# Kernel tuning notes

Hardware: AMD Instinct MI355X
Metric: run time of the kernel (lower is better)

Reference implementation:

```python
import jax, jax.numpy as jnp
import numpy as np

N, A, OBS, H, E, ITERS = 2000, 16, 64, 128, 16000, 8


def _init_linear(key, din, dout):
    kw, kb = jax.random.split(key)
    s = 1.0 / np.sqrt(din)
    W = jax.random.uniform(kw, (dout, din), minval=-s, maxval=s, dtype=jnp.float32)
    b = jax.random.uniform(kb, (dout,), minval=-s, maxval=s, dtype=jnp.float32)
    return W, b


def setup_inputs() -> dict:
    key = jax.random.key(0)
    ks = jax.random.split(key, 20)
    x = jax.random.normal(ks[0], (N, OBS), dtype=jnp.float32)
    prev_action = jax.random.normal(ks[1], (N, A), dtype=jnp.float32)
    state = jax.random.normal(ks[2], (1, N, H), dtype=jnp.float32)
    # edges: unique-ish random pairs with i < j (no self loops)
    rng = np.random.default_rng(0)
    ei = rng.integers(0, N - 1, size=E)
    ej = rng.integers(ei + 1, N)
    edges = jnp.asarray(np.stack([ei, ej], axis=1), dtype=jnp.int32)
    # GRU params (torch layout: rows = [r; z; n])
    s = 1.0 / np.sqrt(H)
    gru_wih = jax.random.uniform(ks[3], (3 * H, OBS + A), minval=-s, maxval=s, dtype=jnp.float32)
    gru_whh = jax.random.uniform(ks[4], (3 * H, H), minval=-s, maxval=s, dtype=jnp.float32)
    gru_bih = jax.random.uniform(ks[5], (3 * H,), minval=-s, maxval=s, dtype=jnp.float32)
    gru_bhh = jax.random.uniform(ks[6], (3 * H,), minval=-s, maxval=s, dtype=jnp.float32)
    # utility MLP: [H, 256, 256, A]
    uW0, ub0 = _init_linear(ks[7], H, 256)
    uW1, ub1 = _init_linear(ks[8], 256, 256)
    uW2, ub2 = _init_linear(ks[9], 256, A)
    # payoff MLP: [2H, H, 256, 256, A, A*A]  (faithful to source's dim-list reuse)
    pW0, pb0 = _init_linear(ks[10], 2 * H, H)
    pW1, pb1 = _init_linear(ks[11], H, 256)
    pW2, pb2 = _init_linear(ks[12], 256, 256)
    pW3, pb3 = _init_linear(ks[13], 256, A)
    pW4, pb4 = _init_linear(ks[14], A, A * A)
    return dict(x=x, prev_action=prev_action, state=state, edges=edges,
                gru_wih=gru_wih, gru_whh=gru_whh, gru_bih=gru_bih, gru_bhh=gru_bhh,
                uW0=uW0, ub0=ub0, uW1=uW1, ub1=ub1, uW2=uW2, ub2=ub2,
                pW0=pW0, pb0=pb0, pW1=pW1, pb1=pb1, pW2=pW2, pb2=pb2,
                pW3=pW3, pb3=pb3, pW4=pW4, pb4=pb4)


def _mlp(x, params):
    n = len(params)
    for i, (W, b) in enumerate(params):
        x = x @ W.T + b
        if i < n - 1:
            x = jax.nn.relu(x)
    return x


def _gru_step(inp, h, wih, whh, bih, bhh):
    gi = inp @ wih.T + bih          # [N, 3H]
    gh = h @ whh.T + bhh            # [N, 3H]
    gir, giz, gin = jnp.split(gi, 3, axis=-1)
    ghr, ghz, ghn = jnp.split(gh, 3, axis=-1)
    r = jax.nn.sigmoid(gir + ghr)
    z = jax.nn.sigmoid(giz + ghz)
    n = jnp.tanh(gin + r * ghn)
    return (1.0 - z) * n + z * h


def _message_passing(u, p, ei, ej):
    """u: [N,A] differentiable, p: [E,A,A] differentiable.
    Messages are computed under stop_gradient (torch.no_grad in source);
    Q of the per-iteration greedy action is differentiable in u, p."""
    u_sg = jax.lax.stop_gradient(u)
    p_sg = jax.lax.stop_gradient(p)
    node_idx = jnp.arange(N)
    edge_idx = jnp.arange(E)

    def step(carry, _):
        M, q_max, opt_a = carry            # M[recv, send, A]
        S = M.sum(axis=1)                  # [N, A] total incoming per node
        base_i = u_sg[ei] + S[ei] - M[ei, ej]   # [E, A] indexed by a_i
        base_j = u_sg[ej] + S[ej] - M[ej, ei]   # [E, A] indexed by a_j
        # message i -> j: max over a_i of (p[e,ai,aj] + base_i[ai])
        msg_to_j = (p_sg + base_i[:, :, None]).max(axis=1)   # [E, A]
        msg_to_j = msg_to_j - msg_to_j.mean(axis=-1, keepdims=True)
        # message j -> i (source reduces over dim 0 = a_i; replicated faithfully)
        msg_to_i = (p_sg + base_j[:, None, :]).max(axis=1)   # [E, A]
        msg_to_i = msg_to_i - msg_to_i.mean(axis=-1, keepdims=True)
        M = M.at[ej, ei].set(msg_to_j).at[ei, ej].set(msg_to_i)
        # greedy action per node
        a_idx = jnp.argmax(u_sg + M.sum(axis=1), axis=-1)    # [N]
        q_real = u[node_idx, a_idx].sum() + p[edge_idx, a_idx[ei], a_idx[ej]].sum()
        better = q_real > q_max
        q_max = jnp.where(better, q_real, q_max)
        a_onehot = jax.nn.one_hot(a_idx, A, dtype=u.dtype)
        opt_a = jnp.where(better, a_onehot, opt_a)
        return (M, q_max, opt_a), None

    M0 = jnp.zeros((N, N, A), dtype=u.dtype)
    q0 = jnp.zeros((), dtype=u.dtype)
    a0 = jnp.zeros((N, A), dtype=u.dtype)
    (M, q_max, opt_a), _ = jax.lax.scan(step, (M0, q0, a0), None, length=ITERS)
    return opt_a, q_max


def reference(x, prev_action, state, edges,
              gru_wih, gru_whh, gru_bih, gru_bhh,
              uW0, ub0, uW1, ub1, uW2, ub2,
              pW0, pb0, pW1, pb1, pW2, pb2, pW3, pb3, pW4, pb4):
    ei, ej = edges[:, 0], edges[:, 1]
    enc_in = jnp.concatenate([x, prev_action], axis=-1)        # [N, OBS+A]
    h = _gru_step(enc_in, state[0], gru_wih, gru_whh, gru_bih, gru_bhh)  # [N, H]
    state_out = h.reshape(1, 1, N, H)
    u_params = [(uW0, ub0), (uW1, ub1), (uW2, ub2)]
    p_params = [(pW0, pb0), (pW1, pb1), (pW2, pb2), (pW3, pb3), (pW4, pb4)]
    u = _mlp(h, u_params) / N                                  # [N, A]
    s_ij = jnp.concatenate([h[ei], h[ej]], axis=-1)            # [E, 2H]
    s_ji = jnp.concatenate([h[ej], h[ei]], axis=-1)
    p_ij = _mlp(s_ij, p_params).reshape(E, A, A) / E
    p_ji = _mlp(s_ji, p_params).reshape(E, A, A) / E
    p = 0.5 * (p_ij + p_ji)                                    # [E, A, A]
    a, q_max = _message_passing(u, p, ei, ej)
    return (a, q_max, u[None], p, state_out)
```

## Files before the change

### kernel.cpp

```cpp
#include <hip/hip_runtime.h>
#include <math.h>

#define N_NODES 2000
#define NA 16
#define NOBS 64
#define NH 128
#define NE 16000
#define NITERS 8

#define WS_MSG       0
#define WS_FLAGS     300000
#define WS_Q         512000
#define WS_SBUF      512016
#define WS_AIDX      800016
#define WS_W         816016
#define WS_PT        832016
#define WS_GIT       (WS_PT + 4000000)
#define WS_GHT       (WS_GIT + 30720)
#define WS_WB        4928016
#define WS_UW0T      (WS_WB + 0)
#define WS_UWCAT     (WS_WB + 32768)
#define WS_UW1T      (WS_WB + 65536)
#define WS_UW2T      (WS_WB + 131072)
#define WS_CAB       (WS_WB + 241664)

#define F16_W1H 0
#define F16_W1L 32768
#define F16_W2H 65536
#define F16_W2L 131072
#define F16_W3H 196608
#define F16_W3L 200704
#define F16_W4H 204800
#define F16_W4L 212992

#define NBLK 500

typedef _Float16 half8 __attribute__((ext_vector_type(8)));
typedef float f32x4 __attribute__((ext_vector_type(4)));

__global__ __launch_bounds__(256) void setup_kernel(
    float* __restrict__ ws, const int* __restrict__ edges,
    const float* __restrict__ uW0, const float* __restrict__ uW1,
    const float* __restrict__ uW2, const float* __restrict__ pW0,
    const float* __restrict__ pW1, const float* __restrict__ pW2,
    const float* __restrict__ pW3, const float* __restrict__ pW4,
    const float* __restrict__ gwih, const float* __restrict__ gwhh)
{
    if (blockIdx.x >= 1024) {
        int e = (blockIdx.x - 1024) * 256 + threadIdx.x;
        if (e < NE) {
            int i = edges[2 * e], j = edges[2 * e + 1];
            ((int*)(ws + WS_PT))[i * N_NODES + j] = -1;
        }
        return;
    }
    const int total = 341904;
    for (int idx = blockIdx.x * 256 + threadIdx.x; idx < total;
         idx += 1024 * 256) {
        if (idx < 16) {
            ws[WS_Q + idx] = 0.f;
        } else {
            int t = idx - 16;
            if (t < 135168) {
                float v;
                if (t < 32768) {
                    int k = t / 256, o = t % 256;
                    v = uW0[o * 128 + k];
                } else if (t < 65536) {
                    int q = t - 32768, k = q / 256, o = q % 256;
                    v = (o < 128) ? pW0[o * 256 + k]
                                  : pW0[(o - 128) * 256 + 128 + k];
                } else if (t < 131072) {
                    int q = t - 65536, k = q / 256, o = q % 256;
                    v = uW1[o * 256 + k];
                } else {
                    int q = t - 131072, k = q / 16, o = q % 16;
                    v = uW2[o * 256 + k];
                }
                ws[WS_WB + t] = v;
            } else if (t < 215056) {
                int q = t - 135168;
                if (q < 30720) {
                    int k4 = q / 1536, r = q % 1536, g = r >> 2, c = r & 3;
                    ws[WS_GIT + q] = gwih[g * 80 + 4 * k4 + c];
                } else if (q < 79872) {
                    int q2 = q - 30720;
                    int k4 = q2 / 1536, r = q2 % 1536, g = r >> 2, c = r & 3;
                    ws[WS_GHT + q2] = gwhh[g * 128 + 4 * k4 + c];
                }
            } else if (t < 325648) {
                int q = t - 215056;
                if (q >= 110592) continue;
                _Float16* fw = (_Float16*)ws;
                float v; int hoff, loff;
                if (q < 32768) {
                    v = pW1[q]; hoff = F16_W1H + q; loff = F16_W1L + q;
                } else if (q < 98304) {
                    int z = q - 32768; v = pW2[z];
                    hoff = F16_W2H + z; loff = F16_W2L + z;
                } else if (q < 102400) {
                    int z = q - 98304; v = pW3[z];
                    hoff = F16_W3H + z; loff = F16_W3L + z;
                } else {
                    int z = q - 102400; int n = z >> 5, kk = z & 31;
                    v = (kk < 16) ? pW4[n * 16 + kk] : 0.f;
                    hoff = F16_W4H + z; loff = F16_W4L + z;
                }
                _Float16 hv = (_Float16)v;
                fw[hoff] = hv;
                fw[loff] = (_Float16)(v - (float)hv);
            } else {
                int qf = t - 325648;
                ((int*)(ws + WS_FLAGS))[qf] = 0;
            }
        }
    }
}

__global__ __launch_bounds__(256) void gru_kernel(
    const float* __restrict__ x, const float* __restrict__ pa,
    const float* __restrict__ st, const float* __restrict__ wihT,
    const float* __restrict__ whhT, const float* __restrict__ bih,
    const float* __restrict__ bhh, float* __restrict__ h_out,
    const int* __restrict__ edges, int* __restrict__ owner)
{
    if (blockIdx.x >= 250) {
        int e = (blockIdx.x - 250) * 256 + threadIdx.x;
        if (e < NE) {
            int i = edges[2 * e], j = edges[2 * e + 1];
            atomicMax(&owner[i * N_NODES + j], e);
        }
        return;
    }
    __shared__ float enc[8][80];
    __shared__ float hp[8][128];
    __shared__ float gi[8][384];
    __shared__ float gh[8][384];
    const int tid = threadIdx.x;
    const int n0 = blockIdx.x * 8;

    for (int idx = tid; idx < 8 * 80; idx += 256) {
        int r = idx / 80, c = idx % 80;
        enc[r][c] = (c < 64) ? x[(n0 + r) * 64 + c] : pa[(n0 + r) * 16 + (c - 64)];
    }
    for (int idx = tid; idx < 8 * 128; idx += 256) {
        int r = idx >> 7, c = idx & 127;
        hp[r][c] = st[(n0 + r) * 128 + c];
    }
    __syncthreads();

    for (int idx = tid; idx < 8 * 384; idx += 256) {
        int g = idx % 384, r = idx / 384;
        float s1 = bih[g];
        #pragma unroll 5
        for (int k4 = 0; k4 < 20; ++k4) {
            const float4 ev = *(const float4*)&enc[r][4 * k4];
            const float4 wv = *(const float4*)&wihT[k4 * 1536 + g * 4];
            s1 = fmaf(ev.x, wv.x, fmaf(ev.y, wv.y, fmaf(ev.z, wv.z, fmaf(ev.w, wv.w, s1))));
        }
        gi[r][g] = s1;
        float s2 = bhh[g];
        #pragma unroll 8
        for (int k4 = 0; k4 < 32; ++k4) {
            const float4 hv = *(const float4*)&hp[r][4 * k4];
            const float4 wv = *(const float4*)&whhT[k4 * 1536 + g * 4];
            s2 = fmaf(hv.x, wv.x, fmaf(hv.y, wv.y, fmaf(hv.z, wv.z, fmaf(hv.w, wv.w, s2))));
        }
        gh[r][g] = s2;
    }
    __syncthreads();

    for (int idx = tid; idx < 8 * 128; idx += 256) {
        int r = idx >> 7, c = idx & 127;
        float rr = 1.f / (1.f + expf(-(gi[r][c] + gh[r][c])));
        float zz = 1.f / (1.f + expf(-(gi[r][128 + c] + gh[r][128 + c])));
        float nn = tanhf(gi[r][256 + c] + rr * gh[r][256 + c]);
        h_out[(n0 + r) * 128 + c] = (1.f - zz) * nn + zz * hp[r][c];
    }
}

__global__ __launch_bounds__(256) void umlp_kernel(
    const float* __restrict__ h, const float* __restrict__ w0t,
    const float* __restrict__ b0, const float* __restrict__ w1t,
    const float* __restrict__ b1, const float* __restrict__ w2t,
    const float* __restrict__ b2, const float* __restrict__ wcat,
    float* __restrict__ u_out, float* __restrict__ Sbuf,
    float* __restrict__ cab, const int* __restrict__ edges,
    const int* __restrict__ owner, int* __restrict__ wflag)
{
    if (blockIdx.x >= 500) {
        int e = (blockIdx.x - 500) * 256 + threadIdx.x;
        if (e < NE) {
            int i = edges[2 * e], j = edges[2 * e + 1];
            wflag[e] = (owner[i * N_NODES + j] == e) ? 1 : 0;
        }
        return;
    }
    __shared__ float A[8][128];
    __shared__ float B[8][256];
    const int tid = threadIdx.x;
    const bool is_cab = blockIdx.x >= 250;
    const int n0 = (is_cab ? blockIdx.x - 250 : blockIdx.x) * 8;

    for (int idx = tid; idx < 8 * 128; idx += 256) {
        int r = idx >> 7, c = idx & 127;
        A[r][c] = h[(n0 + r) * 128 + c];
    }
    __syncthreads();

    if (is_cab) {
        const int o = tid;
        const float* wp = wcat + o;
        float wA[4], wB[4];
        #pragma unroll
        for (int c = 0; c < 4; ++c) wA[c] = wp[c * 256];
        float acc[8];
        #pragma unroll
        for (int r = 0; r < 8; ++r) acc[r] = 0.f;
        for (int k4 = 0; k4 < 32; k4 += 2) {
            #pragma unroll
            for (int c = 0; c < 4; ++c) wB[c] = wp[(4 * (k4 + 1) + c) * 256];
            #pragma unroll
            for (int r = 0; r < 8; ++r) {
                const float4 av = *(const float4*)&A[r][4 * k4];
                acc[r] = fmaf(av.x, wA[0], fmaf(av.y, wA[1], fmaf(av.z, wA[2], fmaf(av.w, wA[3], acc[r]))));
            }
            #pragma unroll
            for (int c = 0; c < 4; ++c) wA[c] = wp[(4 * (k4 + 2) + c) * 256];
            #pragma unroll
            for (int r = 0; r < 8; ++r) {
                const float4 av = *(const float4*)&A[r][4 * k4 + 4];
                acc[r] = fmaf(av.x, wB[0], fmaf(av.y, wB[1], fmaf(av.z, wB[2], fmaf(av.w, wB[3], acc[r]))));
            }
        }
        #pragma unroll
        for (int r = 0; r < 8; ++r) cab[(n0 + r) * 256 + o] = acc[r];
        return;
    }

    {
        const int o = tid;
        const float* wp = w0t + o;
        float wA[4], wB[4];
        #pragma unroll
        for (int c = 0; c < 4; ++c) wA[c] = wp[c * 256];
        float acc[8];
        #pragma unroll
        for (int r = 0; r < 8; ++r) acc[r] = b0[o];
        for (int k4 = 0; k4 < 32; k4 += 2) {
            #pragma unroll
            for (int c = 0; c < 4; ++c) wB[c] = wp[(4 * (k4 + 1) + c) * 256];
            #pragma unroll
            for (int r = 0; r < 8; ++r) {
                const float4 av = *(const float4*)&A[r][4 * k4];
                acc[r] = fmaf(av.x, wA[0], fmaf(av.y, wA[1], fmaf(av.z, wA[2], fmaf(av.w, wA[3], acc[r]))));
            }
            #pragma unroll
            for (int c = 0; c < 4; ++c) wA[c] = wp[(4 * (k4 + 2) + c) * 256];
            #pragma unroll
            for (int r = 0; r < 8; ++r) {
                const float4 av = *(const float4*)&A[r][4 * k4 + 4];
                acc[r] = fmaf(av.x, wB[0], fmaf(av.y, wB[1], fmaf(av.z, wB[2], fmaf(av.w, wB[3], acc[r]))));
            }
        }
        #pragma unroll
        for (int r = 0; r < 8; ++r) B[r][o] = fmaxf(acc[r], 0.f);
    }
    __syncthreads();
    {
        const int o = tid;
        const float* wp = w1t + o;
        float wA[4], wB[4];
        #pragma unroll
        for (int c = 0; c < 4; ++c) wA[c] = wp[c * 256];
        float acc[8];
        #pragma unroll
        for (int r = 0; r < 8; ++r) acc[r] = b1[o];
        for (int k4 = 0; k4 < 64; k4 += 2) {
            #pragma unroll
            for (int c = 0; c < 4; ++c) wB[c] = wp[(4 * (k4 + 1) + c) * 256];
            #pragma unroll
            for (int r = 0; r < 8; ++r) {
                const float4 av = *(const float4*)&B[r][4 * k4];
                acc[r] = fmaf(av.x, wA[0], fmaf(av.y, wA[1], fmaf(av.z, wA[2], fmaf(av.w, wA[3], acc[r]))));
            }
            #pragma unroll
            for (int c = 0; c < 4; ++c) wA[c] = wp[(4 * (k4 + 2) + c) * 256];
            #pragma unroll
            for (int r = 0; r < 8; ++r) {
                const float4 av = *(const float4*)&B[r][4 * k4 + 4];
                acc[r] = fmaf(av.x, wB[0], fmaf(av.y, wB[1], fmaf(av.z, wB[2], fmaf(av.w, wB[3], acc[r]))));
            }
        }
        __syncthreads();
        #pragma unroll
        for (int r = 0; r < 8; ++r) B[r][o] = fmaxf(acc[r], 0.f);
    }
    __syncthreads();
    if (tid < 128) {
        int r = tid >> 4, o = tid & 15;
        float acc = b2[o];
        for (int k4 = 0; k4 < 64; ++k4) {
            const float4 av = *(const float4*)&B[r][4 * k4];
            acc = fmaf(av.x, w2t[(4 * k4 + 0) * 16 + o],
                  fmaf(av.y, w2t[(4 * k4 + 1) * 16 + o],
                  fmaf(av.z, w2t[(4 * k4 + 2) * 16 + o],
                  fmaf(av.w, w2t[(4 * k4 + 3) * 16 + o], acc))));
        }
        float val = acc * (1.f / N_NODES);
        int idx = (n0 + r) * 16 + o;
        u_out[idx] = val;
        #pragma unroll
        for (int t = 0; t < NITERS + 1; ++t) Sbuf[t * 32000 + idx] = val;
    }
}

__global__ __launch_bounds__(512, 6) void pmlp_kernel(
    const float* __restrict__ cab, const int* __restrict__ edges,
    const float* __restrict__ b0, const _Float16* __restrict__ fw,
    const float* __restrict__ b1, const float* __restrict__ b2,
    const float* __restrict__ b3, const float* __restrict__ b4,
    float* __restrict__ p_out, float* __restrict__ pT)
{
    __shared__ __align__(16) _Float16 Ah[32][264];
    __shared__ __align__(16) _Float16 Al[32][264];
    __shared__ float C16[32][16];
    __shared__ float redC[2][32][16];
    __shared__ int fi[32], se[32];

    const int tid  = threadIdx.x;
    const int e0   = blockIdx.x * 16;
    const int wid  = tid >> 6;
    const int lane = tid & 63;
    const int lrow = lane & 15;
    const int lgrp = lane >> 4;
    const int koff = 8 * lgrp;

    if (tid < 16) {
        int i = edges[2 * (e0 + tid)], j = edges[2 * (e0 + tid) + 1];
        fi[2 * tid] = i;     se[2 * tid] = j;
        fi[2 * tid + 1] = j; se[2 * tid + 1] = i;
    }
    __syncthreads();

    {
        const int cl = tid & 127;
        const int rh = tid >> 7;
        const float bb = b0[cl];
        #pragma unroll 4
        for (int r = rh * 8; r < rh * 8 + 8; ++r) {
            float v = cab[fi[r] * 256 + cl] + cab[se[r] * 256 + 128 + cl] + bb;
            v = fmaxf(v, 0.f);
            _Float16 hv = (_Float16)v;
            Ah[r][cl] = hv;
            Al[r][cl] = (_Float16)(v - (float)hv);
        }
    }
    __syncthreads();

    f32x4 acc[2][2];

    #pragma unroll
    for (int mt = 0; mt < 2; ++mt)
        #pragma unroll
        for (int nt = 0; nt < 2; ++nt) acc[mt][nt] = (f32x4){0.f, 0.f, 0.f, 0.f};
    #pragma unroll
    for (int ks = 0; ks < 4; ++ks) {
        half8 ah[2], al[2];
        #pragma unroll
        for (int mt = 0; mt < 2; ++mt) {
            ah[mt] = *(const half8*)&Ah[16 * mt + lrow][32 * ks + koff];
            al[mt] = *(const half8*)&Al[16 * mt + lrow][32 * ks + koff];
        }
        #pragma unroll
        for (int nt = 0; nt < 2; ++nt) {
            const int n = 32 * wid + 16 * nt + lrow;
            half8 bh = *(const half8*)(fw + F16_W1H + n * 128 + 32 * ks + koff);
            half8 bl = *(const half8*)(fw + F16_W1L + n * 128 + 32 * ks + koff);
            #pragma unroll
            for (int mt = 0; mt < 2; ++mt) {
                acc[mt][nt] = __builtin_amdgcn_mfma_f32_16x16x32_f16(ah[mt], bh, acc[mt][nt], 0, 0, 0);
                acc[mt][nt] = __builtin_amdgcn_mfma_f32_16x16x32_f16(ah[mt], bl, acc[mt][nt], 0, 0, 0);
                acc[mt][nt] = __builtin_amdgcn_mfma_f32_16x16x32_f16(al[mt], bh, acc[mt][nt], 0, 0, 0);
            }
        }
    }
    __syncthreads();
    #pragma unroll
    for (int nt = 0; nt < 2; ++nt) {
        const int col = 32 * wid + 16 * nt + lrow;
        const float bv = b1[col];
        #pragma unroll
        for (int mt = 0; mt < 2; ++mt) {
            #pragma unroll
            for (int r = 0; r < 4; ++r) {
                const int row = 16 * mt + 4 * lgrp + r;
                float v = fmaxf(acc[mt][nt][r] + bv, 0.f);
                _Float16 hv = (_Float16)v;
                Ah[row][col] = hv;
                Al[row][col] = (_Float16)(v - (float)hv);
            }
        }
    }
    __syncthreads();

    #pragma unroll
    for (int mt = 0; mt < 2; ++mt)
        #pragma unroll
        for (int nt = 0; nt < 2; ++nt) acc[mt][nt] = (f32x4){0.f, 0.f, 0.f, 0.f};
    for (int ks = 0; ks < 8; ++ks) {
        half8 ah[2], al[2];
        #pragma unroll
        for (int mt = 0; mt < 2; ++mt) {
            ah[mt] = *(const half8*)&Ah[16 * mt + lrow][32 * ks + koff];
            al[mt] = *(const half8*)&Al[16 * mt + lrow][32 * ks + koff];
        }
        #pragma unroll
        for (int nt = 0; nt < 2; ++nt) {
            const int n = 32 * wid + 16 * nt + lrow;
            half8 bh = *(const half8*)(fw + F16_W2H + n * 256 + 32 * ks + koff);
            half8 bl = *(const half8*)(fw + F16_W2L + n * 256 + 32 * ks + koff);
            #pragma unroll
            for (int mt = 0; mt < 2; ++mt) {
                acc[mt][nt] = __builtin_amdgcn_mfma_f32_16x16x32_f16(ah[mt], bh, acc[mt][nt], 0, 0, 0);
                acc[mt][nt] = __builtin_amdgcn_mfma_f32_16x16x32_f16(ah[mt], bl, acc[mt][nt], 0, 0, 0);
                acc[mt][nt] = __builtin_amdgcn_mfma_f32_16x16x32_f16(al[mt], bh, acc[mt][nt], 0, 0, 0);
            }
        }
    }
    __syncthreads();
    #pragma unroll
    for (int nt = 0; nt < 2; ++nt) {
        const int col = 32 * wid + 16 * nt + lrow;
        const float bv = b2[col];
        #pragma unroll
        for (int mt = 0; mt < 2; ++mt) {
            #pragma unroll
            for (int r = 0; r < 4; ++r) {
                const int row = 16 * mt + 4 * lgrp + r;
                float v = fmaxf(acc[mt][nt][r] + bv, 0.f);
                _Float16 hv = (_Float16)v;
                Ah[row][col] = hv;
                Al[row][col] = (_Float16)(v - (float)hv);
            }
        }
    }
    __syncthreads();

    if (wid < 4) {
        const int mt = wid & 1, kh = wid >> 1;
        f32x4 acc3 = {0.f, 0.f, 0.f, 0.f};
        #pragma unroll
        for (int ks = 4 * kh; ks < 4 * kh + 4; ++ks) {
            half8 ah = *(const half8*)&Ah[16 * mt + lrow][32 * ks + koff];
            half8 al = *(const half8*)&Al[16 * mt + lrow][32 * ks + koff];
            half8 bh = *(const half8*)(fw + F16_W3H + lrow * 256 + 32 * ks + koff);
            half8 bl = *(const half8*)(fw + F16_W3L + lrow * 256 + 32 * ks + koff);
            acc3 = __builtin_amdgcn_mfma_f32_16x16x32_f16(ah, bh, acc3, 0, 0, 0);
            acc3 = __builtin_amdgcn_mfma_f32_16x16x32_f16(ah, bl, acc3, 0, 0, 0);
            acc3 = __builtin_amdgcn_mfma_f32_16x16x32_f16(al, bh, acc3, 0, 0, 0);
        }
        #pragma unroll
        for (int r = 0; r < 4; ++r)
            redC[kh][16 * mt + 4 * lgrp + r][lrow] = acc3[r];
    }
    __syncthreads();
    {
        int r = tid >> 4, o = tid & 15;
        C16[r][o] = fmaxf(redC[0][r][o] + redC[1][r][o] + b3[o], 0.f);
    }
    __syncthreads();

    {
        half8 a4h[2], a4l[2];
        #pragma unroll
        for (int mt = 0; mt < 2; ++mt) {
            half8 hh, ll;
            #pragma unroll
            for (int j = 0; j < 8; ++j) { hh[j] = (_Float16)0.f; ll[j] = (_Float16)0.f; }
            if (lgrp < 2) {
                #pragma unroll
                for (int j = 0; j < 8; ++j) {
                    float v = C16[16 * mt + lrow][8 * lgrp + j];
                    _Float16 hv = (_Float16)v;
                    hh[j] = hv;
                    ll[j] = (_Float16)(v - (float)hv);
                }
            }
            a4h[mt] = hh; a4l[mt] = ll;
        }
        #pragma unroll
        for (int nt = 0; nt < 2; ++nt) {
            const int o = 32 * wid + 16 * nt + lrow;
            const float b4v = b4[o];
            half8 bh = *(const half8*)(fw + F16_W4H + o * 32 + koff);
            half8 bl = *(const half8*)(fw + F16_W4L + o * 32 + koff);
            const int ot = (o & 15) * 16 + (o >> 4);
            #pragma unroll
            for (int mt = 0; mt < 2; ++mt) {
                f32x4 a4 = {0.f, 0.f, 0.f, 0.f};
                a4 = __builtin_amdgcn_mfma_f32_16x16x32_f16(a4h[mt], bh, a4, 0, 0, 0);
                a4 = __builtin_amdgcn_mfma_f32_16x16x32_f16(a4h[mt], bl, a4, 0, 0, 0);
                a4 = __builtin_amdgcn_mfma_f32_16x16x32_f16(a4l[mt], bh, a4, 0, 0, 0);
                const int s0 = 8 * mt + 2 * lgrp;
                float pa = (0.5f * (a4[0] + a4[1]) + b4v) * (1.f / NE);
                float pb = (0.5f * (a4[2] + a4[3]) + b4v) * (1.f / NE);
                p_out[(e0 + s0) * 256 + o] = pa;
                p_out[(e0 + s0 + 1) * 256 + o] = pb;
                pT[(e0 + s0) * 256 + ot] = pa;
                pT[(e0 + s0 + 1) * 256 + ot] = pb;
            }
        }
    }
}

__device__ __forceinline__ void grid_bar(int* flags, int gval)
{
    int* gen8 = flags + NBLK * 32;
    __syncthreads();
    if (blockIdx.x == 0) {
        const int i = threadIdx.x;
        if (i >= 1 && i < NBLK) {
            while (__hip_atomic_load(&flags[i * 32], __ATOMIC_RELAXED,
                                     __HIP_MEMORY_SCOPE_AGENT) < gval)
                __builtin_amdgcn_s_sleep(2);
        }
        __syncthreads();
        if (i < 8)
            __hip_atomic_store(&gen8[i * 32], gval, __ATOMIC_RELAXED,
                               __HIP_MEMORY_SCOPE_AGENT);
    } else {
        if (threadIdx.x == 0) {
            asm volatile("s_waitcnt vmcnt(0)" ::: "memory");
            __hip_atomic_store(&flags[blockIdx.x * 32], gval, __ATOMIC_RELAXED,
                               __HIP_MEMORY_SCOPE_AGENT);
            while (__hip_atomic_load(&gen8[(blockIdx.x & 7) * 32],
                                     __ATOMIC_RELAXED,
                                     __HIP_MEMORY_SCOPE_AGENT) < gval)
                __builtin_amdgcn_s_sleep(2);
        }
        __syncthreads();
    }
}

__global__ __launch_bounds__(512, 4) void mp_fused_kernel(
    const float* __restrict__ u, float* __restrict__ Sbuf,
    const float* __restrict__ pT, const float* __restrict__ p,
    const int* __restrict__ edges, const int* __restrict__ wflag,
    int* __restrict__ aidx, float* __restrict__ q,
    float* __restrict__ a_out, float* __restrict__ q_out,
    int* __restrict__ flags)
{
    const int tid = threadIdx.x;
    const int bid = blockIdx.x;
    const int e   = bid * 32 + (tid >> 4);
    const int L   = tid & 15;

    const int gi = edges[2 * e], gj = edges[2 * e + 1];
    const int wf = wflag[e];
    const float4* pt = (const float4*)(pT + e * 256 + L * 16);
    const float4 p0 = pt[0], p1 = pt[1], p2 = pt[2], p3 = pt[3];
    float pv[16] = {p0.x, p0.y, p0.z, p0.w, p1.x, p1.y, p1.z, p1.w,
                    p2.x, p2.y, p2.z, p2.w, p3.x, p3.y, p3.z, p3.w};
    float vmax = -INFINITY;
    #pragma unroll
    for (int a = 0; a < 16; ++a) vmax = fmaxf(vmax, pv[a]);
    float mold_ij = 0.f, mold_ji = 0.f;

    for (int t = 0; t < NITERS; ++t) {
        const float* uSo = Sbuf + t * 32000;
        float* uSn = Sbuf + (t + 1) * 32000;
        const float bi = uSo[gi * 16 + L] - mold_ij;
        const float bj = uSo[gj * 16 + L] - mold_ji;
        float mj = -INFINITY;
        #pragma unroll
        for (int a = 0; a < 16; ++a)
            mj = fmaxf(mj, pv[a] + __shfl(bi, a, 16));
        float mi = vmax + bj;
        float sj = mj, si = mi;
        #pragma unroll
        for (int off = 1; off < 16; off <<= 1) {
            sj += __shfl_xor(sj, off, 16);
            si += __shfl_xor(si, off, 16);
        }
        mj -= sj * (1.f / 16.f);
        mi -= si * (1.f / 16.f);
        mold_ji = mj;
        mold_ij = mi;
        if (wf) {
            atomicAdd(&uSn[gj * 16 + L], mj);
            atomicAdd(&uSn[gi * 16 + L], mi);
        }
        grid_bar(flags, t + 1);
    }

    if (bid < 288) {
        const int t2 = bid / 36;
        const int r2 = (bid % 36) * 512 + tid;
        const float* Sn = Sbuf + (t2 + 1) * 32000;
        float partial = 0.f;
        if (r2 < N_NODES) {
            int n = r2;
            float bv = Sn[n * 16];
            int best = 0;
            #pragma unroll
            for (int a = 1; a < 16; ++a) {
                float v = Sn[n * 16 + a];
                if (v > bv) { bv = v; best = a; }
            }
            __hip_atomic_store(&aidx[t2 * N_NODES + n], best, __ATOMIC_RELAXED,
                               __HIP_MEMORY_SCOPE_AGENT);
            partial = u[n * 16 + best];
        } else if (r2 < N_NODES + NE) {
            int ee = r2 - N_NODES;
            int ii = edges[2 * ee], jj = edges[2 * ee + 1];
            float bvi = Sn[ii * 16]; int ai = 0;
            #pragma unroll
            for (int a = 1; a < 16; ++a) {
                float v = Sn[ii * 16 + a];
                if (v > bvi) { bvi = v; ai = a; }
            }
            float bvj = Sn[jj * 16]; int aj = 0;
            #pragma unroll
            for (int a = 1; a < 16; ++a) {
                float v = Sn[jj * 16 + a];
                if (v > bvj) { bvj = v; aj = a; }
            }
            partial = p[ee * 256 + ai * 16 + aj];
        }
        #pragma unroll
        for (int off = 1; off < 64; off <<= 1)
            partial += __shfl_xor(partial, off, 64);
        if ((tid & 63) == 0) atomicAdd(&q[t2], partial);
    }
    grid_bar(flags, NITERS + 1);

    const int r = bid * 512 + tid;
    if (r < N_NODES * 16) {
        float cur = 0.f; int best_t = -1;
        #pragma unroll
        for (int t2 = 0; t2 < NITERS; ++t2) {
            float qv = q[t2];
            if (qv > cur) { cur = qv; best_t = t2; }
        }
        int n = r >> 4, c = r & 15;
        float val = 0.f;
        if (best_t >= 0 && aidx[best_t * N_NODES + n] == c) val = 1.f;
        a_out[r] = val;
        if (r == 0) q_out[0] = cur;
    }
}

extern "C" void kernel_launch(void* const* d_in, const int* in_sizes, int n_in,
                              void* d_out, int out_size, void* d_ws, size_t ws_size,
                              hipStream_t stream)
{
    (void)in_sizes; (void)n_in; (void)out_size; (void)ws_size;
    const float* x    = (const float*)d_in[0];
    const float* pa   = (const float*)d_in[1];
    const float* st   = (const float*)d_in[2];
    const int*   edges= (const int*)d_in[3];
    const float* gwih = (const float*)d_in[4];
    const float* gwhh = (const float*)d_in[5];
    const float* gbih = (const float*)d_in[6];
    const float* gbhh = (const float*)d_in[7];
    const float* uW0 = (const float*)d_in[8];  const float* ub0 = (const float*)d_in[9];
    const float* uW1 = (const float*)d_in[10]; const float* ub1 = (const float*)d_in[11];
    const float* uW2 = (const float*)d_in[12]; const float* ub2 = (const float*)d_in[13];
    const float* pW0 = (const float*)d_in[14]; const float* pb0 = (const float*)d_in[15];
    const float* pW1 = (const float*)d_in[16]; const float* pb1 = (const float*)d_in[17];
    const float* pW2 = (const float*)d_in[18]; const float* pb2 = (const float*)d_in[19];
    const float* pW3 = (const float*)d_in[20]; const float* pb3 = (const float*)d_in[21];
    const float* pW4 = (const float*)d_in[22]; const float* pb4 = (const float*)d_in[23];

    float* out   = (float*)d_out;
    float* a_out = out;
    float* q_out = out + 32000;
    float* u_out = out + 32001;
    float* p_out = out + 64001;
    float* h_out = out + 4160001;

    float* ws   = (float*)d_ws;
    float* Sbuf = ws + WS_SBUF;
    float* q    = ws + WS_Q;
    int*   flg  = (int*)(ws + WS_FLAGS);
    int*   aidx = (int*)(ws + WS_AIDX);
    int*   wfl  = (int*)(ws + WS_W);
    float* pT   = ws + WS_PT;
    float* cab  = ws + WS_CAB;
    int*   owner= (int*)(ws + WS_PT);

    setup_kernel<<<1087, 256, 0, stream>>>(ws, edges, uW0, uW1, uW2,
                                           pW0, pW1, pW2, pW3, pW4, gwih, gwhh);
    gru_kernel<<<313, 256, 0, stream>>>(x, pa, st, ws + WS_GIT, ws + WS_GHT,
                                        gbih, gbhh, h_out, edges, owner);
    umlp_kernel<<<563, 256, 0, stream>>>(h_out, ws + WS_UW0T, ub0,
                                         ws + WS_UW1T, ub1, ws + WS_UW2T, ub2,
                                         ws + WS_UWCAT, u_out, Sbuf, cab,
                                         edges, owner, wfl);
    pmlp_kernel<<<NE / 16, 512, 0, stream>>>(cab, edges, pb0,
                                             (const _Float16*)ws,
                                             pb1, pb2, pb3, pb4, p_out, pT);
    mp_fused_kernel<<<NBLK, 512, 0, stream>>>(u_out, Sbuf, pT, p_out,
                                              edges, wfl, aidx, q,
                                              a_out, q_out, flg);
}
```

Baseline: 296.7 us.

## Register-tile GRU gates per column and widen node tiles to 32 in GRU and utility MLP

The GRU kernel now has each thread own one hidden column and accumulate the r, z and n gates for 8 rows in registers. Each weight float4 is reused across those rows, and the shared-memory gi/gh staging plus a sync are gone. The GRU and utility-MLP kernels process 32 nodes per block instead of 8, which cuts repeated weight reads from global memory, and edge-bound guards are added for the ragged last tile. The trade-off is far fewer blocks (63 compute blocks on a large GPU) and higher register pressure from 32-wide accumulators, so occupancy and parallelism may suffer.

```diff
diff --git a/kernel.cpp b/kernel.cpp
--- a/kernel.cpp
+++ b/kernel.cpp
@@ -117,65 +117,85 @@
     }
 }
 
-__global__ __launch_bounds__(256) void gru_kernel(
+__global__ __launch_bounds__(512) void gru_kernel(
     const float* __restrict__ x, const float* __restrict__ pa,
     const float* __restrict__ st, const float* __restrict__ wihT,
     const float* __restrict__ whhT, const float* __restrict__ bih,
     const float* __restrict__ bhh, float* __restrict__ h_out,
     const int* __restrict__ edges, int* __restrict__ owner)
 {
-    if (blockIdx.x >= 250) {
-        int e = (blockIdx.x - 250) * 256 + threadIdx.x;
+    if (blockIdx.x >= 63) {
+        int e = (blockIdx.x - 63) * 512 + threadIdx.x;
         if (e < NE) {
             int i = edges[2 * e], j = edges[2 * e + 1];
             atomicMax(&owner[i * N_NODES + j], e);
         }
         return;
     }
-    __shared__ float enc[8][80];
-    __shared__ float hp[8][128];
-    __shared__ float gi[8][384];
-    __shared__ float gh[8][384];
+    __shared__ float enc[32][80];
+    __shared__ float hp[32][128];
     const int tid = threadIdx.x;
-    const int n0 = blockIdx.x * 8;
-
-    for (int idx = tid; idx < 8 * 80; idx += 256) {
+    const int n0 = blockIdx.x * 32;
+
+    for (int idx = tid; idx < 32 * 80; idx += 512) {
         int r = idx / 80, c = idx % 80;
-        enc[r][c] = (c < 64) ? x[(n0 + r) * 64 + c] : pa[(n0 + r) * 16 + (c - 64)];
-    }
-    for (int idx = tid; idx < 8 * 128; idx += 256) {
+        int n = (n0 + r < N_NODES) ? n0 + r : N_NODES - 1;
+        enc[r][c] = (c < 64) ? x[n * 64 + c] : pa[n * 16 + (c - 64)];
+    }
+    for (int idx = tid; idx < 32 * 128; idx += 512) {
         int r = idx >> 7, c = idx & 127;
-        hp[r][c] = st[(n0 + r) * 128 + c];
-    }
-    __syncthreads();
-
-    for (int idx = tid; idx < 8 * 384; idx += 256) {
-        int g = idx % 384, r = idx / 384;
-        float s1 = bih[g];
-        #pragma unroll 5
-        for (int k4 = 0; k4 < 20; ++k4) {
-            const float4 ev = *(const float4*)&enc[r][4 * k4];
-            const float4 wv = *(const float4*)&wihT[k4 * 1536 + g * 4];
-            s1 = fmaf(ev.x, wv.x, fmaf(ev.y, wv.y, fmaf(ev.z, wv.z, fmaf(ev.w, wv.w, s1))));
-        }
-        gi[r][g] = s1;
-        float s2 = bhh[g];
-        #pragma unroll 8
-        for (int k4 = 0; k4 < 32; ++k4) {
-            const float4 hv = *(const float4*)&hp[r][4 * k4];
-            const float4 wv = *(const float4*)&whhT[k4 * 1536 + g * 4];
-            s2 = fmaf(hv.x, wv.x, fmaf(hv.y, wv.y, fmaf(hv.z, wv.z, fmaf(hv.w, wv.w, s2))));
-        }
-        gh[r][g] = s2;
-    }
-    __syncthreads();
-
-    for (int idx = tid; idx < 8 * 128; idx += 256) {
-        int r = idx >> 7, c = idx & 127;
-        float rr = 1.f / (1.f + expf(-(gi[r][c] + gh[r][c])));
-        float zz = 1.f / (1.f + expf(-(gi[r][128 + c] + gh[r][128 + c])));
-        float nn = tanhf(gi[r][256 + c] + rr * gh[r][256 + c]);
-        h_out[(n0 + r) * 128 + c] = (1.f - zz) * nn + zz * hp[r][c];
+        int n = (n0 + r < N_NODES) ? n0 + r : N_NODES - 1;
+        hp[r][c] = st[n * 128 + c];
+    }
+    __syncthreads();
+
+    const int c  = tid & 127;
+    const int r0 = (tid >> 7) * 8;
+    float accR[8], accZ[8], accNi[8], accNh[8];
+    const float bR  = bih[c] + bhh[c];
+    const float bZ  = bih[c + 128] + bhh[c + 128];
+    const float bNi = bih[c + 256];
+    const float bNh = bhh[c + 256];
+    #pragma unroll
+    for (int r = 0; r < 8; ++r) {
+        accR[r] = bR; accZ[r] = bZ; accNi[r] = bNi; accNh[r] = bNh;
+    }
+
+    #pragma unroll 4
+    for (int k4 = 0; k4 < 20; ++k4) {
+        const float4 wr = *(const float4*)&wihT[k4 * 1536 + c * 4];
+        const float4 wz = *(const float4*)&wihT[k4 * 1536 + (c + 128) * 4];
+        const float4 wn = *(const float4*)&wihT[k4 * 1536 + (c + 256) * 4];
+        #pragma unroll
+        for (int r = 0; r < 8; ++r) {
+            const float4 ev = *(const float4*)&enc[r0 + r][4 * k4];
+            accR[r]  = fmaf(ev.x, wr.x, fmaf(ev.y, wr.y, fmaf(ev.z, wr.z, fmaf(ev.w, wr.w, accR[r]))));
+            accZ[r]  = fmaf(ev.x, wz.x, fmaf(ev.y, wz.y, fmaf(ev.z, wz.z, fmaf(ev.w, wz.w, accZ[r]))));
+            accNi[r] = fmaf(ev.x, wn.x, fmaf(ev.y, wn.y, fmaf(ev.z, wn.z, fmaf(ev.w, wn.w, accNi[r]))));
+        }
+    }
+    #pragma unroll 4
+    for (int k4 = 0; k4 < 32; ++k4) {
+        const float4 wr = *(const float4*)&whhT[k4 * 1536 + c * 4];
+        const float4 wz = *(const float4*)&whhT[k4 * 1536 + (c + 128) * 4];
+        const float4 wn = *(const float4*)&whhT[k4 * 1536 + (c + 256) * 4];
+        #pragma unroll
+        for (int r = 0; r < 8; ++r) {
+            const float4 hv = *(const float4*)&hp[r0 + r][4 * k4];
+            accR[r]  = fmaf(hv.x, wr.x, fmaf(hv.y, wr.y, fmaf(hv.z, wr.z, fmaf(hv.w, wr.w, accR[r]))));
+            accZ[r]  = fmaf(hv.x, wz.x, fmaf(hv.y, wz.y, fmaf(hv.z, wz.z, fmaf(hv.w, wz.w, accZ[r]))));
+            accNh[r] = fmaf(hv.x, wn.x, fmaf(hv.y, wn.y, fmaf(hv.z, wn.z, fmaf(hv.w, wn.w, accNh[r]))));
+        }
+    }
+    #pragma unroll
+    for (int r = 0; r < 8; ++r) {
+        int n = n0 + r0 + r;
+        if (n < N_NODES) {
+            float rr = 1.f / (1.f + expf(-accR[r]));
+            float zz = 1.f / (1.f + expf(-accZ[r]));
+            float nn = tanhf(accNi[r] + rr * accNh[r]);
+            h_out[n * 128 + c] = (1.f - zz) * nn + zz * hp[r0 + r][c];
+        }
     }
 }
 
@@ -188,23 +208,24 @@
     float* __restrict__ cab, const int* __restrict__ edges,
     const int* __restrict__ owner, int* __restrict__ wflag)
 {
-    if (blockIdx.x >= 500) {
-        int e = (blockIdx.x - 500) * 256 + threadIdx.x;
+    if (blockIdx.x >= 126) {
+        int e = (blockIdx.x - 126) * 256 + threadIdx.x;
         if (e < NE) {
             int i = edges[2 * e], j = edges[2 * e + 1];
             wflag[e] = (owner[i * N_NODES + j] == e) ? 1 : 0;
         }
         return;
     }
-    __shared__ float A[8][128];
-    __shared__ float B[8][256];
+    __shared__ float A[32][128];
+    __shared__ float B[32][256];
     const int tid = threadIdx.x;
-    const bool is_cab = blockIdx.x >= 250;
-    const int n0 = (is_cab ? blockIdx.x - 250 : blockIdx.x) * 8;
-
-    for (int idx = tid; idx < 8 * 128; idx += 256) {
+    const bool is_cab = blockIdx.x >= 63;
+    const int n0 = (is_cab ? blockIdx.x - 63 : blockIdx.x) * 32;
+
+    for (int idx = tid; idx < 32 * 128; idx += 256) {
         int r = idx >> 7, c = idx & 127;
-        A[r][c] = h[(n0 + r) * 128 + c];
+        int n = (n0 + r < N_NODES) ? n0 + r : N_NODES - 1;
+        A[r][c] = h[n * 128 + c];
     }
     __syncthreads();
 
@@ -214,27 +235,28 @@
         float wA[4], wB[4];
         #pragma unroll
         for (int c = 0; c < 4; ++c) wA[c] = wp[c * 256];
-        float acc[8];
-        #pragma unroll
-        for (int r = 0; r < 8; ++r) acc[r] = 0.f;
+        float acc[32];
+        #pragma unroll
+        for (int r = 0; r < 32; ++r) acc[r] = 0.f;
         for (int k4 = 0; k4 < 32; k4 += 2) {
             #pragma unroll
             for (int c = 0; c < 4; ++c) wB[c] = wp[(4 * (k4 + 1) + c) * 256];
             #pragma unroll
-            for (int r = 0; r < 8; ++r) {
+            for (int r = 0; r < 32; ++r) {
                 const float4 av = *(const float4*)&A[r][4 * k4];
                 acc[r] = fmaf(av.x, wA[0], fmaf(av.y, wA[1], fmaf(av.z, wA[2], fmaf(av.w, wA[3], acc[r]))));
             }
             #pragma unroll
             for (int c = 0; c < 4; ++c) wA[c] = wp[(4 * (k4 + 2) + c) * 256];
             #pragma unroll
-            for (int r = 0; r < 8; ++r) {
+            for (int r = 0; r < 32; ++r) {
                 const float4 av = *(const float4*)&A[r][4 * k4 + 4];
                 acc[r] = fmaf(av.x, wB[0], fmaf(av.y, wB[1], fmaf(av.z, wB[2], fmaf(av.w, wB[3], acc[r]))));
             }
         }
         #pragma unroll
-        for (int r = 0; r < 8; ++r) cab[(n0 + r) * 256 + o] = acc[r];
+        for (int r = 0; r < 32; ++r)
+            if (n0 + r < N_NODES) cab[(n0 + r) * 256 + o] = acc[r];
         return;
     }
 
@@ -244,27 +266,27 @@
         float wA[4], wB[4];
         #pragma unroll
         for (int c = 0; c < 4; ++c) wA[c] = wp[c * 256];
-        float acc[8];
-        #pragma unroll
-        for (int r = 0; r < 8; ++r) acc[r] = b0[o];
+        float acc[32];
+        #pragma unroll
+        for (int r = 0; r < 32; ++r) acc[r] = b0[o];
         for (int k4 = 0; k4 < 32; k4 += 2) {
             #pragma unroll
             for (int c = 0; c < 4; ++c) wB[c] = wp[(4 * (k4 + 1) + c) * 256];
             #pragma unroll
-            for (int r = 0; r < 8; ++r) {
+            for (int r = 0; r < 32; ++r) {
                 const float4 av = *(const float4*)&A[r][4 * k4];
                 acc[r] = fmaf(av.x, wA[0], fmaf(av.y, wA[1], fmaf(av.z, wA[2], fmaf(av.w, wA[3], acc[r]))));
             }
             #pragma unroll
             for (int c = 0; c < 4; ++c) wA[c] = wp[(4 * (k4 + 2) + c) * 256];
             #pragma unroll
-            for (int r = 0; r < 8; ++r) {
+            for (int r = 0; r < 32; ++r) {
                 const float4 av = *(const float4*)&A[r][4 * k4 + 4];
                 acc[r] = fmaf(av.x, wB[0], fmaf(av.y, wB[1], fmaf(av.z, wB[2], fmaf(av.w, wB[3], acc[r]))));
             }
         }
         #pragma unroll
-        for (int r = 0; r < 8; ++r) B[r][o] = fmaxf(acc[r], 0.f);
+        for (int r = 0; r < 32; ++r) B[r][o] = fmaxf(acc[r], 0.f);
     }
     __syncthreads();
     {
@@ -273,32 +295,32 @@
         float wA[4], wB[4];
         #pragma unroll
         for (int c = 0; c < 4; ++c) wA[c] = wp[c * 256];
-        float acc[8];
-        #pragma unroll
-        for (int r = 0; r < 8; ++r) acc[r] = b1[o];
+        float acc[32];
+        #pragma unroll
+        for (int r = 0; r < 32; ++r) acc[r] = b1[o];
         for (int k4 = 0; k4 < 64; k4 += 2) {
             #pragma unroll
             for (int c = 0; c < 4; ++c) wB[c] = wp[(4 * (k4 + 1) + c) * 256];
             #pragma unroll
-            for (int r = 0; r < 8; ++r) {
+            for (int r = 0; r < 32; ++r) {
                 const float4 av = *(const float4*)&B[r][4 * k4];
                 acc[r] = fmaf(av.x, wA[0], fmaf(av.y, wA[1], fmaf(av.z, wA[2], fmaf(av.w, wA[3], acc[r]))));
             }
             #pragma unroll
             for (int c = 0; c < 4; ++c) wA[c] = wp[(4 * (k4 + 2) + c) * 256];
             #pragma unroll
-            for (int r = 0; r < 8; ++r) {
+            for (int r = 0; r < 32; ++r) {
                 const float4 av = *(const float4*)&B[r][4 * k4 + 4];
                 acc[r] = fmaf(av.x, wB[0], fmaf(av.y, wB[1], fmaf(av.z, wB[2], fmaf(av.w, wB[3], acc[r]))));
             }
         }
         __syncthreads();
         #pragma unroll
-        for (int r = 0; r < 8; ++r) B[r][o] = fmaxf(acc[r], 0.f);
-    }
-    __syncthreads();
-    if (tid < 128) {
-        int r = tid >> 4, o = tid & 15;
+        for (int r = 0; r < 32; ++r) B[r][o] = fmaxf(acc[r], 0.f);
+    }
+    __syncthreads();
+    for (int idx = tid; idx < 512; idx += 256) {
+        int r = idx >> 4, o = idx & 15;
         float acc = b2[o];
         for (int k4 = 0; k4 < 64; ++k4) {
             const float4 av = *(const float4*)&B[r][4 * k4];
@@ -307,11 +329,13 @@
                   fmaf(av.z, w2t[(4 * k4 + 2) * 16 + o],
                   fmaf(av.w, w2t[(4 * k4 + 3) * 16 + o], acc))));
         }
-        float val = acc * (1.f / N_NODES);
-        int idx = (n0 + r) * 16 + o;
-        u_out[idx] = val;
-        #pragma unroll
-        for (int t = 0; t < NITERS + 1; ++t) Sbuf[t * 32000 + idx] = val;
+        if (n0 + r < N_NODES) {
+            float val = acc * (1.f / N_NODES);
+            int oidx = (n0 + r) * 16 + o;
+            u_out[oidx] = val;
+            #pragma unroll
+            for (int t = 0; t < NITERS + 1; ++t) Sbuf[t * 32000 + oidx] = val;
+        }
     }
 }
 
@@ -692,9 +716,9 @@
 
     setup_kernel<<<1087, 256, 0, stream>>>(ws, edges, uW0, uW1, uW2,
                                            pW0, pW1, pW2, pW3, pW4, gwih, gwhh);
-    gru_kernel<<<313, 256, 0, stream>>>(x, pa, st, ws + WS_GIT, ws + WS_GHT,
-                                        gbih, gbhh, h_out, edges, owner);
-    umlp_kernel<<<563, 256, 0, stream>>>(h_out, ws + WS_UW0T, ub0,
+    gru_kernel<<<95, 512, 0, stream>>>(x, pa, st, ws + WS_GIT, ws + WS_GHT,
+                                       gbih, gbhh, h_out, edges, owner);
+    umlp_kernel<<<189, 256, 0, stream>>>(h_out, ws + WS_UW0T, ub0,
                                          ws + WS_UW1T, ub1, ws + WS_UW2T, ub2,
                                          ws + WS_UWCAT, u_out, Sbuf, cab,
                                          edges, owner, wfl);
```

Result: slower. 370.0 us (+24.7%).
